# Performance work log

Hardware: AMD Instinct MI355X
Metric: run time of the kernel (lower is better)

The kernel has to match this reference:

```python
import jax, jax.numpy as jnp
import numpy as np

BN_EPS = 1e-5

def conv3d(x, w, b):
    # standard 3D conv, stride 1, pad 1, NCDHW
    out = jax.lax.conv_general_dilated(x, w, (1, 1, 1), ((1, 1), (1, 1), (1, 1)),
                                       dimension_numbers=('NCDHW', 'OIDHW', 'NCDHW'))
    return out + b[None, :, None, None, None]

def batchnorm(x, gamma, beta):
    # training-mode BN over (B, D, H, W) per channel
    mu = x.mean(axis=(0, 2, 3, 4), keepdims=True)
    var = x.var(axis=(0, 2, 3, 4), keepdims=True)
    g = gamma[None, :, None, None, None]
    b = beta[None, :, None, None, None]
    return g * (x - mu) * jax.lax.rsqrt(var + BN_EPS) + b

def deform_conv3d(x, offset, weight, cpg):
    # x: [B,C,D,H,W]; offset: [B, G*27*3, D,H,W] with layout [B,G,27,(d,h,w),D,H,W]
    # weight: [C_out, C_in, 3,3,3]; kernel 3, stride 1, pad 1 -> same spatial size
    B, C, D, H, W = x.shape
    G = C // cpg
    off = offset.reshape(B, G, 27, 3, D, H, W)
    k = jnp.arange(27)
    kd = (k // 9 - 1).astype(x.dtype).reshape(1, 1, 27, 1, 1, 1)
    kh = ((k // 3) % 3 - 1).astype(x.dtype).reshape(1, 1, 27, 1, 1, 1)
    kw = (k % 3 - 1).astype(x.dtype).reshape(1, 1, 27, 1, 1, 1)
    gd = jnp.arange(D, dtype=x.dtype).reshape(1, 1, 1, D, 1, 1)
    gh = jnp.arange(H, dtype=x.dtype).reshape(1, 1, 1, 1, H, 1)
    gw = jnp.arange(W, dtype=x.dtype).reshape(1, 1, 1, 1, 1, W)
    # fractional sampling positions per (batch, group, tap, voxel): [B,G,27,D,H,W]
    pd = gd + kd + off[:, :, :, 0]
    ph = gh + kh + off[:, :, :, 1]
    pw = gw + kw + off[:, :, :, 2]
    d0 = jnp.floor(pd); h0 = jnp.floor(ph); w0 = jnp.floor(pw)
    fd = pd - d0; fh = ph - h0; fw = pw - w0
    d0i = d0.astype(jnp.int32); h0i = h0.astype(jnp.int32); w0i = w0.astype(jnp.int32)
    xg = x.reshape(B, G, cpg, D * H * W)
    N = 27 * D * H * W
    acc = jnp.zeros((B, G, cpg, 27, D, H, W), x.dtype)
    for dd in (0, 1):
        for hh in (0, 1):
            for ww in (0, 1):
                di = d0i + dd; hi = h0i + hh; wi = w0i + ww
                wgt = ((fd if dd else 1.0 - fd) * (fh if hh else 1.0 - fh)
                       * (fw if ww else 1.0 - fw))
                valid = ((di >= 0) & (di < D) & (hi >= 0) & (hi < H)
                         & (wi >= 0) & (wi < W))  # zero padding outside
                dic = jnp.clip(di, 0, D - 1)
                hic = jnp.clip(hi, 0, H - 1)
                wic = jnp.clip(wi, 0, W - 1)
                idx = ((dic * H + hic) * W + wic).reshape(B, G, 1, N)
                vals = jnp.take_along_axis(xg, jnp.broadcast_to(idx, (B, G, cpg, N)), axis=3)
                vals = vals.reshape(B, G, cpg, 27, D, H, W)
                acc = acc + (wgt * valid)[:, :, None] * vals
    wr = weight.reshape(weight.shape[0], G, cpg, 27)
    return jnp.einsum('bgckdhw,ogck->bodhw', acc, wr)

def setup_inputs() -> dict:
    key = jax.random.key(0)
    ks = jax.random.split(key, 8)
    B, C, D, H, W = 2, 64, 8, 32, 32
    cpg = 8
    Coff = (C // cpg) * 3 * 27  # 648
    fan = 1.0 / np.sqrt(C * 27)
    x = jax.random.normal(ks[0], (B, C, D, H, W), jnp.float32)
    w_off1 = jax.random.normal(ks[1], (Coff, C, 3, 3, 3), jnp.float32) * 0.01
    b_off1 = jnp.zeros((Coff,), jnp.float32)
    w1 = jax.random.normal(ks[2], (C, C, 3, 3, 3), jnp.float32) * fan
    g1 = jnp.ones((C,), jnp.float32)
    be1 = jnp.zeros((C,), jnp.float32)
    w_off2 = jax.random.normal(ks[3], (Coff, C, 3, 3, 3), jnp.float32) * 0.01
    b_off2 = jnp.zeros((Coff,), jnp.float32)
    w2 = jax.random.normal(ks[4], (C, C, 3, 3, 3), jnp.float32) * fan
    g2 = jnp.ones((C,), jnp.float32)
    be2 = jnp.zeros((C,), jnp.float32)
    return {'x': x, 'w_off1': w_off1, 'b_off1': b_off1, 'w1': w1, 'g1': g1,
            'be1': be1, 'w_off2': w_off2, 'b_off2': b_off2, 'w2': w2,
            'g2': g2, 'be2': be2, 'cpg': cpg}

def reference(x, w_off1, b_off1, w1, g1, be1, w_off2, b_off2, w2, g2, be2, cpg):
    off1 = conv3d(x, w_off1, b_off1)
    out = deform_conv3d(x, off1, w1, cpg)
    out = jax.nn.relu(batchnorm(out, g1, be1))
    off2 = conv3d(x, w_off2, b_off2)  # note: offsets computed from x, as in source
    out = deform_conv3d(out, off2, w2, cpg)
    out = batchnorm(out, g2, be2) + x
    out = jax.nn.relu(out)
    return (out, off1, off2)
```

## Files before the change

### kernel.cpp

```cpp
#include <hip/hip_runtime.h>
#include <stdint.h>

typedef unsigned short u16;
typedef __attribute__((ext_vector_type(8))) short bf16x8;
typedef __attribute__((ext_vector_type(4))) float f32x4;

#define DEV static __device__ __forceinline__

#define BB    2
#define CC    64
#define DDD   8
#define HHH   32
#define WWW   32
#define DHW   8192
#define MTOT  16384
#define GG    8
#define KTOT  1728
#define NOFF  1296
#define NOFFP 1408
#define COFF  648

#define OFF1_ELEM (BB*CC*DHW)
#define OFF2_ELEM (OFF1_ELEM + BB*COFF*DHW)

#define XCL_OFF   0ull
#define YCL_OFF   2097152ull
#define WOFF_OFF  4194304ull
#define W1_OFF    9060352ull
#define W2_OFF    9281536ull
#define C1_OFF    9502720ull
#define C2_OFF    13697024ull
#define ST1_OFF   17891328ull
#define ST2_OFF   17891840ull
#define ZPG_OFF   17892352ull
#define PART_OFF  17892608ull

DEV float bf2f(u16 u){ union { uint32_t i; float f; } v; v.i = ((uint32_t)u) << 16; return v.f; }
DEV u16 f2bf(float f){ union { float f; uint32_t i; } v; v.f = f;
  uint32_t r = v.i + 0x7fffu + ((v.i >> 16) & 1u); return (u16)(r >> 16); }

DEV void gld16(const void* g, void* l){
  __builtin_amdgcn_global_load_lds((const __attribute__((address_space(1))) void*)g,
                                   (__attribute__((address_space(3))) void*)l, 16, 0, 0);
}

#define PRE0 (BB*CC*DHW)
#define PRE1 (PRE0 + NOFFP*KTOT)
#define PRE2 (PRE1 + CC*KTOT)
#define PRE3 (PRE2 + CC*KTOT)
#define PRETOT (PRE3 + 128)

__global__ void k_prep(const float* __restrict__ x,
                       const float* __restrict__ wo1, const float* __restrict__ wo2,
                       const float* __restrict__ w1, const float* __restrict__ w2,
                       u16* __restrict__ xcl, u16* __restrict__ woff,
                       u16* __restrict__ w1b, u16* __restrict__ w2b,
                       u16* __restrict__ zpg)
{
  int idx = blockIdx.x * 256 + threadIdx.x;
  if (idx < PRE0) {
    int p = idx & (DHW - 1);
    int c = (idx >> 13) & 63;
    int b = idx >> 19;
    xcl[(size_t)(b * DHW + p) * CC + c] = f2bf(x[idx]);
  } else if (idx < PRE1) {
    int j = idx - PRE0;
    int k = j % KTOT, n = j / KTOT;
    int tap = k >> 6, cin = k & 63;
    float v = 0.f;
    if (n < NOFF) {
      const float* w = (n < COFF) ? wo1 : wo2;
      int nn = (n < COFF) ? n : n - COFF;
      v = w[(size_t)nn * KTOT + cin * 27 + tap];
    }
    woff[j] = f2bf(v);
  } else if (idx < PRE2) {
    int j = idx - PRE1;
    int k = j % KTOT, n = j / KTOT;
    int tap = k >> 6, cin = k & 63;
    w1b[j] = f2bf(w1[(size_t)n * KTOT + cin * 27 + tap]);
  } else if (idx < PRE3) {
    int j = idx - PRE2;
    int k = j % KTOT, n = j / KTOT;
    int tap = k >> 6, cin = k & 63;
    w2b[j] = f2bf(w2[(size_t)n * KTOT + cin * 27 + tap]);
  } else if (idx < PRETOT) {
    zpg[idx - PRE3] = 0;
  }
}

__global__ __launch_bounds__(256) void k_gemm_off(
    const u16* __restrict__ xcl, const u16* __restrict__ woff,
    const float* __restrict__ boff1, const float* __restrict__ boff2,
    float* __restrict__ dout, const u16* __restrict__ zpg)
{
  __shared__ u16 Al[128 * 64];
  __shared__ u16 Bl[128 * 64];
  const int tid = threadIdx.x;
  const int wv = tid >> 6, lane = tid & 63;
  const int m0 = blockIdx.x * 128;
  const int n0 = blockIdx.y * 128;
  const int lr = lane >> 3, lc = lane & 7;
  const int lcs = (lc ^ lr) << 3;
  const int b  = m0 >> 13;
  const int p0 = m0 & (DHW - 1);
  int ad[4], ah[4], aw[4];
  #pragma unroll
  for (int i = 0; i < 4; ++i) {
    int p = p0 + wv * 32 + i * 8 + lr;
    ad[i] = p >> 10; ah[i] = (p >> 5) & 31; aw[i] = p & 31;
  }
  const size_t xb = (size_t)b * DHW * CC;

  f32x4 acc[4][4] = {};
  const int wm = wv >> 1, wn = wv & 1;
  const int r16 = lane & 15, q = lane >> 4;
  const int rs = r16 & 7;
  const int nbase = n0 + wn * 64;
  const int jlim = (nbase >= NOFF) ? 0 : ((NOFF - nbase >= 64) ? 4 : ((NOFF - nbase + 15) >> 4));

  for (int t = 0; t < 27; ++t) {
    int kd = t / 9 - 1, kh = (t / 3) % 3 - 1, kw = t % 3 - 1;
    #pragma unroll
    for (int i = 0; i < 4; ++i) {
      int d2 = ad[i] + kd, h2 = ah[i] + kh, w2 = aw[i] + kw;
      bool ok = ((unsigned)d2 < DDD) & ((unsigned)h2 < HHH) & ((unsigned)w2 < WWW);
      const u16* src = ok ? (xcl + xb + (size_t)((d2 << 10) + (h2 << 5) + w2) * CC + lcs)
                          : zpg;
      gld16(src, &Al[(wv * 32 + i * 8) * 64]);
    }
    #pragma unroll
    for (int i = 0; i < 4; ++i) {
      int r = wv * 32 + i * 8 + lr;
      const u16* src = woff + (size_t)(n0 + r) * KTOT + t * 64 + lcs;
      gld16(src, &Bl[(wv * 32 + i * 8) * 64]);
    }
    __syncthreads();
    #pragma unroll
    for (int kk = 0; kk < 2; ++kk) {
      const int cs = ((kk * 4 + q) ^ rs) << 3;
      bf16x8 af[4];
      #pragma unroll
      for (int i = 0; i < 4; ++i)
        af[i] = *(const bf16x8*)&Al[(wm * 64 + i * 16 + r16) * 64 + cs];
      #pragma unroll
      for (int j = 0; j < 4; ++j) {
        if (j < jlim) {
          bf16x8 bfr = *(const bf16x8*)&Bl[(wn * 64 + j * 16 + r16) * 64 + cs];
          #pragma unroll
          for (int i = 0; i < 4; ++i)
            acc[i][j] = __builtin_amdgcn_mfma_f32_16x16x32_bf16(af[i], bfr, acc[i][j], 0, 0, 0);
        }
      }
    }
    __syncthreads();
  }

  float biasj[4]; int ncj[4];
  #pragma unroll
  for (int j = 0; j < 4; ++j) {
    int nc = n0 + wn * 64 + j * 16 + r16;
    ncj[j] = nc;
    biasj[j] = (nc < NOFF) ? ((nc < COFF) ? boff1[nc] : boff2[nc - COFF]) : 0.f;
  }
  #pragma unroll
  for (int i = 0; i < 4; ++i) {
    int mrow = m0 + wm * 64 + i * 16 + q * 4;
    int bb = mrow >> 13, p = mrow & (DHW - 1);
    #pragma unroll
    for (int j = 0; j < 4; ++j) {
      int nc = ncj[j];
      if (nc < NOFF) {
        int ch = (nc < COFF) ? nc : nc - COFF;
        size_t base = (nc < COFF) ? (size_t)OFF1_ELEM : (size_t)OFF2_ELEM;
        f32x4 v = acc[i][j] + biasj[j];
        *(f32x4*)(dout + base + ((size_t)(bb * COFF + ch)) * DHW + p) = v;
      }
    }
  }
}

__global__ __launch_bounds__(256) void k_deform(
    const u16* __restrict__ src, const float* __restrict__ offs,
    const u16* __restrict__ wB, float* __restrict__ cdst,
    const u16* __restrict__ zpg)
{
  __shared__ u16 Al[2 * 16 * 64];
  __shared__ u16 Bl[2 * 64 * 64];
  const int tid = threadIdx.x;
  const int wv = tid >> 6, lane = tid & 63;
  const int mrow0 = blockIdx.x * 16;
  const int b  = mrow0 >> 13;
  const int p0 = mrow0 & (DHW - 1);

  const int pl = tid & 15;
  const int g  = (tid >> 4) & 7;
  const int th = tid >> 7;
  const int p  = p0 + pl;
  const int d = p >> 10, h = (p >> 5) & 31, w = p & 31;
  const u16* sb = src + (size_t)b * DHW * CC + g * 8;
  const size_t obase = ((size_t)(b * COFF + g * 81)) * DHW + p;
  u16* awp = &Al[th * 1024 + pl * 64 + ((g ^ (pl & 7)) << 3)];

  const int lr = lane >> 3, lc = lane & 7;
  const int lcs = (lc ^ lr) << 3;

  f32x4 acc = {};
  const int r16 = lane & 15, q = lane >> 4;
  const int rs = r16 & 7;

  for (int ph = 0; ph < 14; ++ph) {
    #pragma unroll
    for (int i = 0; i < 4; ++i) {
      int tb = 2 * ph + (i >> 1);
      int row = (i & 1) * 32 + wv * 8 + lr;
      const u16* s = (tb < 27) ? (wB + (size_t)row * KTOT + tb * 64 + lcs) : zpg;
      gld16(s, &Bl[(i >> 1) * 4096 + (((i & 1) * 32 + wv * 8) * 64)]);
    }
    {
      int t = 2 * ph + th;
      float a8[8] = {0.f,0.f,0.f,0.f,0.f,0.f,0.f,0.f};
      if (t < 27) {
        int kd = t / 9 - 1, kh = (t / 3) % 3 - 1, kw = t % 3 - 1;
        size_t ob = obase + (size_t)(t * 3) * DHW;
        float pd = (float)(d + kd) + offs[ob];
        float phh = (float)(h + kh) + offs[ob + DHW];
        float pw = (float)(w + kw) + offs[ob + 2 * DHW];
        float fd0 = floorf(pd), fh0 = floorf(phh), fw0 = floorf(pw);
        float fd = pd - fd0, fh = phh - fh0, fw = pw - fw0;
        int d0 = (int)fd0, h0 = (int)fh0, w0 = (int)fw0;
        #pragma unroll
        for (int dd = 0; dd < 2; ++dd) {
          float wd = dd ? fd : 1.f - fd;
          int di = d0 + dd;
          #pragma unroll
          for (int hh = 0; hh < 2; ++hh) {
            float wh = hh ? fh : 1.f - fh;
            int hi = h0 + hh;
            #pragma unroll
            for (int ww = 0; ww < 2; ++ww) {
              int wi = w0 + ww;
              if (((unsigned)di < DDD) && ((unsigned)hi < HHH) && ((unsigned)wi < WWW)) {
                float wgt = wd * wh * (ww ? fw : 1.f - fw);
                bf16x8 v = *(const bf16x8*)(sb + (size_t)((di << 10) + (hi << 5) + wi) * CC);
                #pragma unroll
                for (int c = 0; c < 8; ++c) a8[c] += wgt * bf2f((u16)v[c]);
              }
            }
          }
        }
      }
      union { bf16x8 v; u16 u[8]; } o;
      #pragma unroll
      for (int c = 0; c < 8; ++c) o.u[c] = f2bf(a8[c]);
      *(bf16x8*)awp = o.v;
    }
    __syncthreads();
    #pragma unroll
    for (int tt = 0; tt < 2; ++tt) {
      #pragma unroll
      for (int kk = 0; kk < 2; ++kk) {
        const int cs = ((kk * 4 + q) ^ rs) << 3;
        bf16x8 af = *(const bf16x8*)&Al[tt * 1024 + r16 * 64 + cs];
        bf16x8 bf_ = *(const bf16x8*)&Bl[tt * 4096 + (wv * 16 + r16) * 64 + cs];
        acc = __builtin_amdgcn_mfma_f32_16x16x32_bf16(af, bf_, acc, 0, 0, 0);
      }
    }
    __syncthreads();
  }

  {
    int nc = wv * 16 + r16;
    int mr = mrow0 + q * 4;
    #pragma unroll
    for (int r = 0; r < 4; ++r)
      cdst[(size_t)(mr + r) * CC + nc] = acc[r];
  }
}

__global__ void k_bnpart(const float* __restrict__ c, float* __restrict__ part)
{
  int k = blockIdx.x, tid = threadIdx.x;
  int ch = tid & 63, sub = tid >> 6;
  float s = 0.f, s2 = 0.f;
  for (int mm = sub; mm < 64; mm += 4) {
    float v = c[(size_t)(k * 64 + mm) * CC + ch];
    s += v; s2 += v * v;
  }
  __shared__ float sh[4][128];
  sh[sub][ch] = s; sh[sub][64 + ch] = s2;
  __syncthreads();
  if (tid < 128)
    part[(size_t)k * 128 + tid] = sh[0][tid] + sh[1][tid] + sh[2][tid] + sh[3][tid];
}

__global__ void k_bnfin(const float* __restrict__ part, const float* __restrict__ gamma,
                        const float* __restrict__ beta, float* __restrict__ stats)
{
  int n = threadIdx.x;
  float S = 0.f, S2 = 0.f;
  for (int k = 0; k < 256; ++k) {
    S  += part[(size_t)k * 128 + n];
    S2 += part[(size_t)k * 128 + 64 + n];
  }
  float mu = S / (float)MTOT;
  float var = S2 / (float)MTOT - mu * mu;
  float sc = gamma[n] / sqrtf(var + 1e-5f);
  stats[n] = sc;
  stats[64 + n] = beta[n] - mu * sc;
}

__global__ void k_apply1(const float* __restrict__ c1, const float* __restrict__ st,
                         u16* __restrict__ ycl)
{
  int idx = blockIdx.x * 256 + threadIdx.x;
  if (idx >= MTOT * CC) return;
  int n = idx & 63;
  float v = st[n] * c1[idx] + st[64 + n];
  ycl[idx] = f2bf(fmaxf(v, 0.f));
}

__global__ void k_apply2(const float* __restrict__ c2, const float* __restrict__ st,
                         const float* __restrict__ x, float* __restrict__ out)
{
  int idx = blockIdx.x * 256 + threadIdx.x;
  if (idx >= BB * CC * DHW) return;
  int p = idx & (DHW - 1);
  int n = (idx >> 13) & 63;
  int b = idx >> 19;
  float v = st[n] * c2[(size_t)(b * DHW + p) * CC + n] + st[64 + n] + x[idx];
  out[idx] = fmaxf(v, 0.f);
}

extern "C" void kernel_launch(void* const* d_in, const int* in_sizes, int n_in,
                              void* d_out, int out_size, void* d_ws, size_t ws_size,
                              hipStream_t stream)
{
  (void)in_sizes; (void)n_in; (void)out_size; (void)ws_size;
  const float* x      = (const float*)d_in[0];
  const float* w_off1 = (const float*)d_in[1];
  const float* b_off1 = (const float*)d_in[2];
  const float* w1     = (const float*)d_in[3];
  const float* g1     = (const float*)d_in[4];
  const float* be1    = (const float*)d_in[5];
  const float* w_off2 = (const float*)d_in[6];
  const float* b_off2 = (const float*)d_in[7];
  const float* w2     = (const float*)d_in[8];
  const float* g2     = (const float*)d_in[9];
  const float* be2    = (const float*)d_in[10];

  char* ws = (char*)d_ws;
  u16*   xcl  = (u16*)(ws + XCL_OFF);
  u16*   ycl  = (u16*)(ws + YCL_OFF);
  u16*   woff = (u16*)(ws + WOFF_OFF);
  u16*   w1b  = (u16*)(ws + W1_OFF);
  u16*   w2b  = (u16*)(ws + W2_OFF);
  float* c1   = (float*)(ws + C1_OFF);
  float* c2   = (float*)(ws + C2_OFF);
  float* st1  = (float*)(ws + ST1_OFF);
  float* st2  = (float*)(ws + ST2_OFF);
  u16*   zpg  = (u16*)(ws + ZPG_OFF);
  float* part = (float*)(ws + PART_OFF);
  float* out  = (float*)d_out;

  k_prep<<<(PRETOT + 255) / 256, 256, 0, stream>>>(
      x, w_off1, w_off2, w1, w2, xcl, woff, w1b, w2b, zpg);

  k_gemm_off<<<dim3(MTOT / 128, NOFFP / 128), 256, 0, stream>>>(
      xcl, woff, b_off1, b_off2, out, zpg);

  k_deform<<<MTOT / 16, 256, 0, stream>>>(xcl, out + OFF1_ELEM, w1b, c1, zpg);
  k_bnpart<<<256, 256, 0, stream>>>(c1, part);
  k_bnfin<<<1, 64, 0, stream>>>(part, g1, be1, st1);
  k_apply1<<<(MTOT * CC) / 256, 256, 0, stream>>>(c1, st1, ycl);

  k_deform<<<MTOT / 16, 256, 0, stream>>>(ycl, out + OFF2_ELEM, w2b, c2, zpg);
  k_bnpart<<<256, 256, 0, stream>>>(c2, part);
  k_bnfin<<<1, 64, 0, stream>>>(part, g2, be2, st2);
  k_apply2<<<(BB*CC*DHW) / 256, 256, 0, stream>>>(c2, st2, x, out);
}
```

Before: 259.9 us.

## Double-buffer LDS in offset GEMM and deform kernels, rebalance BN reduction

Adds double buffering of shared-memory tiles to the offset GEMM and both deformable-conv kernels, so the next tap's global loads and bilinear sampling are issued before the current tap's MFMAs run, and one barrier per iteration is dropped. The deform kernel's thread-to-(voxel,group) mapping is changed so each wave handles a fixed tap half. The offset GEMM drops the jlim guard and always runs all MFMAs, including on padded columns. BN partial reduction uses fewer, larger blocks, and the finalize kernel spreads its work over 128 threads with a shared-memory combine. Doubled LDS use may lower occupancy.

```diff
diff --git a/kernel.cpp b/kernel.cpp
--- a/kernel.cpp
+++ b/kernel.cpp
@@ -94,8 +94,8 @@
     const float* __restrict__ boff1, const float* __restrict__ boff2,
     float* __restrict__ dout, const u16* __restrict__ zpg)
 {
-  __shared__ u16 Al[128 * 64];
-  __shared__ u16 Bl[128 * 64];
+  __shared__ u16 Al[2 * 128 * 64];
+  __shared__ u16 Bl[2 * 128 * 64];
   const int tid = threadIdx.x;
   const int wv = tid >> 6, lane = tid & 63;
   const int m0 = blockIdx.x * 128;
@@ -116,44 +116,53 @@
   const int wm = wv >> 1, wn = wv & 1;
   const int r16 = lane & 15, q = lane >> 4;
   const int rs = r16 & 7;
-  const int nbase = n0 + wn * 64;
-  const int jlim = (nbase >= NOFF) ? 0 : ((NOFF - nbase >= 64) ? 4 : ((NOFF - nbase + 15) >> 4));
-
-  for (int t = 0; t < 27; ++t) {
+
+  auto stage = [&](int buf, int t) {
     int kd = t / 9 - 1, kh = (t / 3) % 3 - 1, kw = t % 3 - 1;
+    u16* Ab = &Al[buf * 8192];
+    u16* Bb = &Bl[buf * 8192];
     #pragma unroll
     for (int i = 0; i < 4; ++i) {
       int d2 = ad[i] + kd, h2 = ah[i] + kh, w2 = aw[i] + kw;
       bool ok = ((unsigned)d2 < DDD) & ((unsigned)h2 < HHH) & ((unsigned)w2 < WWW);
       const u16* src = ok ? (xcl + xb + (size_t)((d2 << 10) + (h2 << 5) + w2) * CC + lcs)
                           : zpg;
-      gld16(src, &Al[(wv * 32 + i * 8) * 64]);
+      gld16(src, &Ab[(wv * 32 + i * 8) * 64]);
     }
     #pragma unroll
     for (int i = 0; i < 4; ++i) {
       int r = wv * 32 + i * 8 + lr;
       const u16* src = woff + (size_t)(n0 + r) * KTOT + t * 64 + lcs;
-      gld16(src, &Bl[(wv * 32 + i * 8) * 64]);
-    }
-    __syncthreads();
+      gld16(src, &Bb[(wv * 32 + i * 8) * 64]);
+    }
+  };
+
+  stage(0, 0);
+  __syncthreads();
+  int cur = 0;
+
+  for (int t = 0; t < 27; ++t) {
+    if (t < 26) stage(cur ^ 1, t + 1);
+    const u16* Ab = &Al[cur * 8192];
+    const u16* Bb = &Bl[cur * 8192];
     #pragma unroll
     for (int kk = 0; kk < 2; ++kk) {
       const int cs = ((kk * 4 + q) ^ rs) << 3;
-      bf16x8 af[4];
+      bf16x8 af[4], bfr[4];
       #pragma unroll
       for (int i = 0; i < 4; ++i)
-        af[i] = *(const bf16x8*)&Al[(wm * 64 + i * 16 + r16) * 64 + cs];
+        af[i] = *(const bf16x8*)&Ab[(wm * 64 + i * 16 + r16) * 64 + cs];
       #pragma unroll
-      for (int j = 0; j < 4; ++j) {
-        if (j < jlim) {
-          bf16x8 bfr = *(const bf16x8*)&Bl[(wn * 64 + j * 16 + r16) * 64 + cs];
-          #pragma unroll
-          for (int i = 0; i < 4; ++i)
-            acc[i][j] = __builtin_amdgcn_mfma_f32_16x16x32_bf16(af[i], bfr, acc[i][j], 0, 0, 0);
-        }
-      }
+      for (int j = 0; j < 4; ++j)
+        bfr[j] = *(const bf16x8*)&Bb[(wn * 64 + j * 16 + r16) * 64 + cs];
+      #pragma unroll
+      for (int i = 0; i < 4; ++i)
+        #pragma unroll
+        for (int j = 0; j < 4; ++j)
+          acc[i][j] = __builtin_amdgcn_mfma_f32_16x16x32_bf16(af[i], bfr[j], acc[i][j], 0, 0, 0);
     }
     __syncthreads();
+    cur ^= 1;
   }
 
   float biasj[4]; int ncj[4];
@@ -185,22 +194,23 @@
     const u16* __restrict__ wB, float* __restrict__ cdst,
     const u16* __restrict__ zpg)
 {
-  __shared__ u16 Al[2 * 16 * 64];
-  __shared__ u16 Bl[2 * 64 * 64];
+  __shared__ u16 Al[2 * 2 * 16 * 64];
+  __shared__ u16 Bl[2 * 2 * 64 * 64];
   const int tid = threadIdx.x;
   const int wv = tid >> 6, lane = tid & 63;
   const int mrow0 = blockIdx.x * 16;
   const int b  = mrow0 >> 13;
   const int p0 = mrow0 & (DHW - 1);
 
-  const int pl = tid & 15;
-  const int g  = (tid >> 4) & 7;
-  const int th = tid >> 7;
+  const int th = wv >> 1;
+  const int pv = wv & 1;
+  const int pl = (lane & 7) + pv * 8;
+  const int g  = lane >> 3;
   const int p  = p0 + pl;
   const int d = p >> 10, h = (p >> 5) & 31, w = p & 31;
   const u16* sb = src + (size_t)b * DHW * CC + g * 8;
   const size_t obase = ((size_t)(b * COFF + g * 81)) * DHW + p;
-  u16* awp = &Al[th * 1024 + pl * 64 + ((g ^ (pl & 7)) << 3)];
+  const int awoff = th * 1024 + pl * 64 + ((g ^ (pl & 7)) << 3);
 
   const int lr = lane >> 3, lc = lane & 7;
   const int lcs = (lc ^ lr) << 3;
@@ -209,64 +219,77 @@
   const int r16 = lane & 15, q = lane >> 4;
   const int rs = r16 & 7;
 
-  for (int ph = 0; ph < 14; ++ph) {
+  auto stageB = [&](int buf, int ph) {
+    u16* Bb = &Bl[buf * 8192];
     #pragma unroll
     for (int i = 0; i < 4; ++i) {
       int tb = 2 * ph + (i >> 1);
       int row = (i & 1) * 32 + wv * 8 + lr;
       const u16* s = (tb < 27) ? (wB + (size_t)row * KTOT + tb * 64 + lcs) : zpg;
-      gld16(s, &Bl[(i >> 1) * 4096 + (((i & 1) * 32 + wv * 8) * 64)]);
-    }
-    {
-      int t = 2 * ph + th;
-      float a8[8] = {0.f,0.f,0.f,0.f,0.f,0.f,0.f,0.f};
-      if (t < 27) {
-        int kd = t / 9 - 1, kh = (t / 3) % 3 - 1, kw = t % 3 - 1;
-        size_t ob = obase + (size_t)(t * 3) * DHW;
-        float pd = (float)(d + kd) + offs[ob];
-        float phh = (float)(h + kh) + offs[ob + DHW];
-        float pw = (float)(w + kw) + offs[ob + 2 * DHW];
-        float fd0 = floorf(pd), fh0 = floorf(phh), fw0 = floorf(pw);
-        float fd = pd - fd0, fh = phh - fh0, fw = pw - fw0;
-        int d0 = (int)fd0, h0 = (int)fh0, w0 = (int)fw0;
+      gld16(s, &Bb[(i >> 1) * 4096 + (((i & 1) * 32 + wv * 8) * 64)]);
+    }
+  };
+
+  auto sample = [&](int buf, int ph) {
+    int t = 2 * ph + th;
+    float a8[8] = {0.f,0.f,0.f,0.f,0.f,0.f,0.f,0.f};
+    if (t < 27) {
+      int kd = t / 9 - 1, kh = (t / 3) % 3 - 1, kw = t % 3 - 1;
+      size_t ob = obase + (size_t)(t * 3) * DHW;
+      float pd = (float)(d + kd) + offs[ob];
+      float phh = (float)(h + kh) + offs[ob + DHW];
+      float pw = (float)(w + kw) + offs[ob + 2 * DHW];
+      float fd0 = floorf(pd), fh0 = floorf(phh), fw0 = floorf(pw);
+      float fd = pd - fd0, fh = phh - fh0, fw = pw - fw0;
+      int d0 = (int)fd0, h0 = (int)fh0, w0 = (int)fw0;
+      #pragma unroll
+      for (int dd = 0; dd < 2; ++dd) {
+        float wd = dd ? fd : 1.f - fd;
+        int di = d0 + dd;
         #pragma unroll
-        for (int dd = 0; dd < 2; ++dd) {
-          float wd = dd ? fd : 1.f - fd;
-          int di = d0 + dd;
+        for (int hh = 0; hh < 2; ++hh) {
+          float wh = hh ? fh : 1.f - fh;
+          int hi = h0 + hh;
           #pragma unroll
-          for (int hh = 0; hh < 2; ++hh) {
-            float wh = hh ? fh : 1.f - fh;
-            int hi = h0 + hh;
-            #pragma unroll
-            for (int ww = 0; ww < 2; ++ww) {
-              int wi = w0 + ww;
-              if (((unsigned)di < DDD) && ((unsigned)hi < HHH) && ((unsigned)wi < WWW)) {
-                float wgt = wd * wh * (ww ? fw : 1.f - fw);
-                bf16x8 v = *(const bf16x8*)(sb + (size_t)((di << 10) + (hi << 5) + wi) * CC);
-                #pragma unroll
-                for (int c = 0; c < 8; ++c) a8[c] += wgt * bf2f((u16)v[c]);
-              }
+          for (int ww = 0; ww < 2; ++ww) {
+            int wi = w0 + ww;
+            if (((unsigned)di < DDD) && ((unsigned)hi < HHH) && ((unsigned)wi < WWW)) {
+              float wgt = wd * wh * (ww ? fw : 1.f - fw);
+              bf16x8 v = *(const bf16x8*)(sb + (size_t)((di << 10) + (hi << 5) + wi) * CC);
+              #pragma unroll
+              for (int c = 0; c < 8; ++c) a8[c] += wgt * bf2f((u16)v[c]);
             }
           }
         }
       }
-      union { bf16x8 v; u16 u[8]; } o;
-      #pragma unroll
-      for (int c = 0; c < 8; ++c) o.u[c] = f2bf(a8[c]);
-      *(bf16x8*)awp = o.v;
-    }
-    __syncthreads();
+    }
+    union { bf16x8 v; u16 u[8]; } o;
+    #pragma unroll
+    for (int c = 0; c < 8; ++c) o.u[c] = f2bf(a8[c]);
+    *(bf16x8*)&Al[buf * 2048 + awoff] = o.v;
+  };
+
+  stageB(0, 0);
+  sample(0, 0);
+  __syncthreads();
+  int cur = 0;
+
+  for (int ph = 0; ph < 14; ++ph) {
+    if (ph < 13) { stageB(cur ^ 1, ph + 1); sample(cur ^ 1, ph + 1); }
+    const u16* Ab = &Al[cur * 2048];
+    const u16* Bb = &Bl[cur * 8192];
     #pragma unroll
     for (int tt = 0; tt < 2; ++tt) {
       #pragma unroll
       for (int kk = 0; kk < 2; ++kk) {
         const int cs = ((kk * 4 + q) ^ rs) << 3;
-        bf16x8 af = *(const bf16x8*)&Al[tt * 1024 + r16 * 64 + cs];
-        bf16x8 bf_ = *(const bf16x8*)&Bl[tt * 4096 + (wv * 16 + r16) * 64 + cs];
+        bf16x8 af = *(const bf16x8*)&Ab[tt * 1024 + r16 * 64 + cs];
+        bf16x8 bf_ = *(const bf16x8*)&Bb[tt * 4096 + (wv * 16 + r16) * 64 + cs];
         acc = __builtin_amdgcn_mfma_f32_16x16x32_bf16(af, bf_, acc, 0, 0, 0);
       }
     }
     __syncthreads();
+    cur ^= 1;
   }
 
   {
@@ -283,8 +306,8 @@
   int k = blockIdx.x, tid = threadIdx.x;
   int ch = tid & 63, sub = tid >> 6;
   float s = 0.f, s2 = 0.f;
-  for (int mm = sub; mm < 64; mm += 4) {
-    float v = c[(size_t)(k * 64 + mm) * CC + ch];
+  for (int mm = sub; mm < 256; mm += 4) {
+    float v = c[(size_t)(k * 256 + mm) * CC + ch];
     s += v; s2 += v * v;
   }
   __shared__ float sh[4][128];
@@ -297,17 +320,19 @@
 __global__ void k_bnfin(const float* __restrict__ part, const float* __restrict__ gamma,
                         const float* __restrict__ beta, float* __restrict__ stats)
 {
-  int n = threadIdx.x;
-  float S = 0.f, S2 = 0.f;
-  for (int k = 0; k < 256; ++k) {
-    S  += part[(size_t)k * 128 + n];
-    S2 += part[(size_t)k * 128 + 64 + n];
-  }
-  float mu = S / (float)MTOT;
-  float var = S2 / (float)MTOT - mu * mu;
-  float sc = gamma[n] / sqrtf(var + 1e-5f);
-  stats[n] = sc;
-  stats[64 + n] = beta[n] - mu * sc;
+  int tid = threadIdx.x;
+  float S = 0.f;
+  for (int k = 0; k < 64; ++k) S += part[(size_t)k * 128 + tid];
+  __shared__ float sh[128];
+  sh[tid] = S;
+  __syncthreads();
+  if (tid < 64) {
+    float mu = sh[tid] / (float)MTOT;
+    float var = sh[64 + tid] / (float)MTOT - mu * mu;
+    float sc = gamma[tid] / sqrtf(var + 1e-5f);
+    stats[tid] = sc;
+    stats[64 + tid] = beta[tid] - mu * sc;
+  }
 }
 
 __global__ void k_apply1(const float* __restrict__ c1, const float* __restrict__ st,
@@ -370,12 +395,12 @@
       xcl, woff, b_off1, b_off2, out, zpg);
 
   k_deform<<<MTOT / 16, 256, 0, stream>>>(xcl, out + OFF1_ELEM, w1b, c1, zpg);
-  k_bnpart<<<256, 256, 0, stream>>>(c1, part);
-  k_bnfin<<<1, 64, 0, stream>>>(part, g1, be1, st1);
+  k_bnpart<<<64, 256, 0, stream>>>(c1, part);
+  k_bnfin<<<1, 128, 0, stream>>>(part, g1, be1, st1);
   k_apply1<<<(MTOT * CC) / 256, 256, 0, stream>>>(c1, st1, ycl);
 
   k_deform<<<MTOT / 16, 256, 0, stream>>>(ycl, out + OFF2_ELEM, w2b, c2, zpg);
-  k_bnpart<<<256, 256, 0, stream>>>(c2, part);
-  k_bnfin<<<1, 64, 0, stream>>>(part, g2, be2, st2);
+  k_bnpart<<<64, 256, 0, stream>>>(c2, part);
+  k_bnfin<<<1, 128, 0, stream>>>(part, g2, be2, st2);
   k_apply2<<<(BB*CC*DHW) / 256, 256, 0, stream>>>(c2, st2, x, out);
 }
```

After: 291.9 us. 12.3% more time.
